# Optimization experiments

Measured on AMD Instinct MI355X. Metric: run time of the kernel, lower is better.

## Reference

```python
import jax, jax.numpy as jnp
import numpy as np

B, T, D, H, K, V, W = 2, 2048, 768, 12, 64, 64, 1024
EPS = 1e-6


def setup_inputs() -> dict:
    key = jax.random.key(0)
    ks = jax.random.split(key, 10)
    std = 0.02
    return {
        "x": jax.random.normal(ks[0], (B, T, D), jnp.float32),
        "gdn_state": jax.random.normal(ks[1], (B, H, K, V), jnp.float32),
        "Wq": jax.random.normal(ks[2], (D, H * K), jnp.float32) * std,
        "Wk": jax.random.normal(ks[3], (D, H * K), jnp.float32) * std,
        "Wv": jax.random.normal(ks[4], (D, H * K), jnp.float32) * std,
        "Wo": jax.random.normal(ks[5], (H * K, D), jnp.float32) * std,
        "Wgq": jax.random.normal(ks[6], (D, H * K), jnp.float32) * std,
        "Wro": jax.random.normal(ks[7], (H * V, D), jnp.float32) * std,
        "Wg": jax.random.normal(ks[8], (D, H), jnp.float32) * std,
        "bg": jnp.full((H,), 1.0, jnp.float32),  # swa_gate_init
        "norm_w": jnp.ones((D,), jnp.float32),
    }


def reference(x, gdn_state, Wq, Wk, Wv, Wo, Wgq, Wro, Wg, bg, norm_w):
    # RMSNorm
    xn = x * jax.lax.rsqrt(jnp.mean(x * x, axis=-1, keepdims=True) + EPS) * norm_w

    def proj(w):  # (B,T,D)@(D,HK) -> (B,H,T,K)
        return (xn @ w).reshape(B, T, H, K).transpose(0, 2, 1, 3)

    q, k, v = proj(Wq), proj(Wk), proj(Wv)
    scale = K ** -0.5

    scores = jnp.einsum("bhqk,bhsk->bhqs", q, k) * scale  # (B,H,T,T)
    i = jnp.arange(T)[:, None]
    j = jnp.arange(T)[None, :]
    allowed = (j <= i) & (j >= i - W)  # causal sliding window
    scores = jnp.where(allowed, scores, -jnp.inf)
    attn = jax.nn.softmax(scores, axis=-1)

    local = jnp.einsum("bhqs,bhsk->bhqk", attn, v)
    local = local.transpose(0, 2, 1, 3).reshape(B, T, H * K) @ Wo  # (B,T,D)

    # GDN state retrieval
    qg = jax.nn.relu((xn @ Wgq).reshape(B, T, H, K).transpose(0, 2, 1, 3))  # (B,H,T,K)
    retrieved = jnp.einsum("bhkv,bhtk->bhtv", gdn_state, qg)  # (B,H,T,V)
    retrieval = retrieved.transpose(0, 2, 1, 3).reshape(B, T, H * V) @ Wro  # (B,T,D)
    gate = jax.nn.sigmoid(xn @ Wg + bg)  # (B,T,H)
    retrieval = jnp.mean(gate, axis=-1, keepdims=True) * retrieval

    return x + local + retrieval
```

## Files before the change

### kernel.cpp

```cpp
#include <hip/hip_runtime.h>
#include <math.h>
#include <stdint.h>

typedef float f32x4 __attribute__((ext_vector_type(4)));
typedef __bf16 bf16x8 __attribute__((ext_vector_type(8)));
typedef __bf16 bf16x4 __attribute__((ext_vector_type(4)));

constexpr int Bc = 2, Tc = 2048, Dc = 768, Hc = 12, Wc = 1024;
#define CEXP 0.18033688011112042f

__device__ __forceinline__ f32x4 mfma_bf16(bf16x8 a, bf16x8 b, f32x4 c) {
    return __builtin_amdgcn_mfma_f32_16x16x32_bf16(a, b, c, 0, 0, 0);
}
__device__ __forceinline__ void gload16(const void* g, void* l) {
    __builtin_amdgcn_global_load_lds(
        (const __attribute__((address_space(1))) uint32_t*)g,
        (__attribute__((address_space(3))) uint32_t*)l, 16, 0, 0);
}
__device__ __forceinline__ uint32_t pack2(float a, float b) {
    union { __bf16 h[2]; uint32_t u; } x;
    x.h[0] = (__bf16)a; x.h[1] = (__bf16)b; return x.u;
}

__global__ __launch_bounds__(256) void k_prep_w(
    const float* __restrict__ Wq, const float* __restrict__ Wk,
    const float* __restrict__ Wv, const float* __restrict__ Wgq,
    const float* __restrict__ Wo, const float* __restrict__ Wro,
    __bf16* __restrict__ wTproj, __bf16* __restrict__ wTout)
{
    __shared__ __bf16 ldsT[64][66];
    const int wsel = blockIdx.y;
    const float* srcs[6] = {Wq, Wk, Wv, Wgq, Wo, Wro};
    const float* src = srcs[wsel];
    __bf16* dst; int dstride, koff;
    if (wsel < 4) { dst = wTproj + (size_t)wsel * Dc * Dc; dstride = Dc;  koff = 0; }
    else if (wsel == 4) { dst = wTout; dstride = 1536; koff = 0; }
    else { dst = wTout; dstride = 1536; koff = 768; }
    const float scale = (wsel == 0) ? CEXP : 1.0f;

    int tile = blockIdx.x;
    int tk = tile % 12, tn = tile / 12;
    int k0 = tk * 64, n0 = tn * 64;
    int i = threadIdx.x, rsub = i >> 4, c4 = i & 15;
#pragma unroll
    for (int rep = 0; rep < 4; ++rep) {
        int row = rep * 16 + rsub;
        float4 v = *(const float4*)(src + (size_t)(k0 + row) * Dc + n0 + c4 * 4);
        ldsT[c4 * 4 + 0][row] = (__bf16)(v.x * scale);
        ldsT[c4 * 4 + 1][row] = (__bf16)(v.y * scale);
        ldsT[c4 * 4 + 2][row] = (__bf16)(v.z * scale);
        ldsT[c4 * 4 + 3][row] = (__bf16)(v.w * scale);
    }
    __syncthreads();
#pragma unroll
    for (int rep = 0; rep < 4; ++rep) {
        int n = rep * 16 + rsub;
        bf16x4 o = *(const bf16x4*)&ldsT[n][c4 * 4];
        *(bf16x4*)(dst + (size_t)(n0 + n) * dstride + koff + k0 + c4 * 4) = o;
    }
}

__global__ __launch_bounds__(256) void k_prep_state(
    const float* __restrict__ st, __bf16* __restrict__ stT)
{
    int idx = blockIdx.x * 256 + threadIdx.x;
    int bh = idx >> 12, kk = (idx >> 6) & 63, vv = idx & 63;
    stT[(size_t)bh * 4096 + vv * 64 + kk] = (__bf16)st[idx];
}

__global__ __launch_bounds__(256) void k_rmsnorm(
    const float* __restrict__ x, const float* __restrict__ norm_w,
    __bf16* __restrict__ xnb)
{
    int row = blockIdx.x, tid = threadIdx.x;
    const float* xr = x + (size_t)row * Dc;
    float4 v = make_float4(0.f, 0.f, 0.f, 0.f);
    float ss = 0.f;
    if (tid < 192) {
        v = ((const float4*)xr)[tid];
        ss = v.x * v.x + v.y * v.y + v.z * v.z + v.w * v.w;
    }
#pragma unroll
    for (int m = 32; m; m >>= 1) ss += __shfl_xor(ss, m, 64);
    __shared__ float red[4];
    if ((tid & 63) == 0) red[tid >> 6] = ss;
    __syncthreads();
    float tot = red[0] + red[1] + red[2] + red[3];
    float rms = rsqrtf(tot * (1.f / 768.f) + 1e-6f);
    if (tid < 192) {
        float4 nw = ((const float4*)norm_w)[tid];
        bf16x4 o;
        o[0] = (__bf16)(v.x * rms * nw.x);
        o[1] = (__bf16)(v.y * rms * nw.y);
        o[2] = (__bf16)(v.z * rms * nw.z);
        o[3] = (__bf16)(v.w * rms * nw.w);
        *(bf16x4*)(xnb + (size_t)row * Dc + tid * 4) = o;
    }
}

__global__ __launch_bounds__(256) void k_gate(
    const __bf16* __restrict__ xnb, const float* __restrict__ Wg,
    const float* __restrict__ bg, float* __restrict__ gmean)
{
    int row = blockIdx.x * 4 + (threadIdx.x >> 6);
    int lane = threadIdx.x & 63;
    const __bf16* xr = xnb + (size_t)row * Dc;
    float p[12];
#pragma unroll
    for (int h = 0; h < 12; ++h) p[h] = 0.f;
    for (int d = lane; d < Dc; d += 64) {
        float xv = (float)xr[d];
        const float* wr = Wg + d * 12;
#pragma unroll
        for (int h = 0; h < 12; ++h) p[h] += xv * wr[h];
    }
#pragma unroll
    for (int h = 0; h < 12; ++h) {
#pragma unroll
        for (int m = 32; m; m >>= 1) p[h] += __shfl_xor(p[h], m, 64);
    }
    if (lane == 0) {
        float s = 0.f;
#pragma unroll
        for (int h = 0; h < 12; ++h) s += 1.f / (1.f + expf(-(p[h] + bg[h])));
        gmean[row] = s * (1.f / 12.f);
    }
}

template <int MODE>
__global__ __launch_bounds__(256) void k_gemm(
    const __bf16* __restrict__ A, const __bf16* __restrict__ BT,
    const float* __restrict__ xres, float* __restrict__ outf,
    __bf16* __restrict__ qb, __bf16* __restrict__ kbf,
    __bf16* __restrict__ vtb, __bf16* __restrict__ qgb)
{
    constexpr int BM = (MODE == 0) ? 128 : 64;
    constexpr int BN = (MODE == 0) ? 128 : 64;
    constexpr int KD = (MODE == 0) ? 768 : 1536;
    constexpr int WM = BM / 2, WN = BN / 2;
    constexpr int MI = WM / 16, NI = WN / 16;
    constexpr int MT = 4096 / BM;
    __shared__ __bf16 As[BM * 32];
    __shared__ __bf16 Bs[BN * 32];
    const int tid = threadIdx.x, w = tid >> 6, lane = tid & 63;
    const int g = lane >> 4, t = lane & 15;
    int id = blockIdx.x, xcd = id & 7, l = id >> 3;
    int nid = xcd * 96 + l;
    int m0 = (nid % MT) * BM, n0 = (nid / MT) * BN;
    const __bf16* Abase = A + (size_t)m0 * KD;
    const __bf16* Bbase = BT + (size_t)n0 * KD;
    const int wrow = (w >> 1) * WM, wcol = (w & 1) * WN;

    f32x4 acc[MI][NI] = {};
    for (int k0 = 0; k0 < KD; k0 += 32) {
#pragma unroll
        for (int c = 0; c < BM / 64; ++c) {
            int chunk = c * 256 + tid, row = chunk >> 2, cix = chunk & 3;
            gload16(Abase + (size_t)row * KD + k0 + cix * 8, As + chunk * 8);
        }
#pragma unroll
        for (int c = 0; c < BN / 64; ++c) {
            int chunk = c * 256 + tid, row = chunk >> 2, cix = chunk & 3;
            gload16(Bbase + (size_t)row * KD + k0 + cix * 8, Bs + chunk * 8);
        }
        __syncthreads();
        bf16x8 af[MI], bfr[NI];
#pragma unroll
        for (int mi = 0; mi < MI; ++mi)
            af[mi] = *(const bf16x8*)(As + (wrow + mi * 16 + t) * 32 + g * 8);
#pragma unroll
        for (int ni = 0; ni < NI; ++ni)
            bfr[ni] = *(const bf16x8*)(Bs + (wcol + ni * 16 + t) * 32 + g * 8);
#pragma unroll
        for (int mi = 0; mi < MI; ++mi)
#pragma unroll
            for (int ni = 0; ni < NI; ++ni)
                acc[mi][ni] = mfma_bf16(af[mi], bfr[ni], acc[mi][ni]);
        __syncthreads();
    }
    const int region = (MODE == 0) ? (n0 / 768) : 0;
#pragma unroll
    for (int mi = 0; mi < MI; ++mi)
#pragma unroll
        for (int ni = 0; ni < NI; ++ni)
#pragma unroll
            for (int r = 0; r < 4; ++r) {
                int grow = m0 + wrow + mi * 16 + g * 4 + r;
                int gcol = n0 + wcol + ni * 16 + t;
                float v = acc[mi][ni][r];
                if (MODE == 1) {
                    size_t idx = (size_t)grow * Dc + gcol;
                    outf[idx] = xres[idx] + v;
                } else {
                    int c = gcol - region * 768;
                    int h = c >> 6, kd = c & 63;
                    int b = grow >> 11, ti = grow & (Tc - 1);
                    if (region == 0)
                        qb[((size_t)(b * Hc + h) * Tc + ti) * 64 + kd] = (__bf16)v;
                    else if (region == 1) {
                        int kds = kd ^ ((ti & 7) << 3);
                        kbf[((size_t)(b * Hc + h) * Tc + ti) * 64 + kds] = (__bf16)v;
                    } else if (region == 2) {
                        int ts = (ti & ~63) | ((ti & 63) ^ ((kd & 7) << 3));
                        vtb[((size_t)(b * Hc + h) * 64 + kd) * Tc + ts] = (__bf16)v;
                    } else
                        qgb[((size_t)(b * Hc + h) * Tc + ti) * 64 + kd] = (__bf16)fmaxf(v, 0.f);
                }
            }
}

__global__ __launch_bounds__(256) void k_attn(
    const __bf16* __restrict__ q, const __bf16* __restrict__ k,
    const __bf16* __restrict__ vt, __bf16* __restrict__ ac)
{
    __shared__ __bf16 Ks[2][64 * 64];
    __shared__ __bf16 Vs[2][64 * 64];
    int id = blockIdx.x, xcd = id & 7, l = id >> 3;
    int nid = xcd * 96 + l;
    int sblk = nid & 31, h = (nid >> 5) % Hc, b = nid / (32 * Hc);
    int tid = threadIdx.x;
    int w = tid >> 6, lane = tid & 63;
    int g = lane >> 4, t = lane & 15;
    int q0 = sblk * 64, qw = q0 + w * 16;
    const __bf16* qb = q + (size_t)(b * Hc + h) * Tc * 64;
    const __bf16* kb = k + (size_t)(b * Hc + h) * Tc * 64;
    const __bf16* vb = vt + (size_t)(b * Hc + h) * 64 * Tc;

    bf16x8 qf0 = *(const bf16x8*)(qb + (size_t)(qw + t) * 64 + g * 8);
    bf16x8 qf1 = *(const bf16x8*)(qb + (size_t)(qw + t) * 64 + 32 + g * 8);

    const int qi = qw + t;
    const int lowB = qi - Wc;
    const int xr = t & 7;

    f32x4 oacc[4] = {};
    float lsum = 0.f;

    const int s_begin = (q0 >= Wc) ? q0 - Wc : 0;
    const int s_endq = q0 + 64;

    auto STAGE = [&](int buf, int s0) {
#pragma unroll
        for (int j = 0; j < 2; ++j) {
            int ch = j * 256 + tid;
            gload16(kb + (size_t)(s0 + (ch >> 3)) * 64 + (ch & 7) * 8,
                    &Ks[buf][ch * 8]);
            gload16(vb + (size_t)(ch >> 3) * Tc + s0 + (ch & 7) * 8,
                    &Vs[buf][ch * 8]);
        }
    };

    STAGE(0, s_begin);
    __syncthreads();
    int cur = 0;
    for (int s0 = s_begin; s0 < s_endq; s0 += 64) {
        if (s0 + 64 < s_endq) STAGE(cur ^ 1, s0 + 64);
        const __bf16* Kt = Ks[cur];
        const __bf16* Vt = Vs[cur];
        f32x4 sc[4];
#pragma unroll
        for (int sub = 0; sub < 4; ++sub) {
            const __bf16* kr = Kt + (sub * 16 + t) * 64;
            bf16x8 kA = *(const bf16x8*)(kr + ((g ^ xr) << 3));
            bf16x8 kB = *(const bf16x8*)(kr + (((g + 4) ^ xr) << 3));
            f32x4 s = {};
            s = mfma_bf16(kA, qf0, s);
            s = mfma_bf16(kB, qf1, s);
            sc[sub] = s;
        }
        float pv[4][4];
#pragma unroll
        for (int sub = 0; sub < 4; ++sub)
#pragma unroll
            for (int r = 0; r < 4; ++r) {
                int kk = s0 + sub * 16 + g * 4 + r;
                float e = exp2f(sc[sub][r]);
                float val = (kk <= qi && kk >= lowB) ? e : 0.f;
                pv[sub][r] = val;
                lsum += val;
            }
#pragma unroll
        for (int ks = 0; ks < 2; ++ks) {
            const float* p0 = pv[ks * 2];
            const float* p1 = pv[ks * 2 + 1];
            uint32_t u0 = pack2(p0[0], p0[1]), u1 = pack2(p0[2], p0[3]);
            uint32_t u2 = pack2(p1[0], p1[1]), u3 = pack2(p1[2], p1[3]);
            int srcA = (g & 1) * 32 + t, srcB = srcA + 16;
            uint32_t a0 = __shfl(u0, srcA, 64), a1 = __shfl(u1, srcA, 64);
            uint32_t a2 = __shfl(u0, srcB, 64), a3 = __shfl(u1, srcB, 64);
            uint32_t c0 = __shfl(u2, srcA, 64), c1 = __shfl(u3, srcA, 64);
            uint32_t c2 = __shfl(u2, srcB, 64), c3 = __shfl(u3, srcB, 64);
            bool lo2 = g < 2;
            union { uint32_t u[4]; bf16x8 v; } pf;
            pf.u[0] = lo2 ? a0 : c0; pf.u[1] = lo2 ? a1 : c1;
            pf.u[2] = lo2 ? a2 : c2; pf.u[3] = lo2 ? a3 : c3;
#pragma unroll
            for (int n = 0; n < 4; ++n) {
                const __bf16* vrow = Vt + (n * 16 + t) * 64;
                bf16x8 vf = *(const bf16x8*)(vrow + ((((ks * 4) + g) ^ xr) << 3));
                oacc[n] = mfma_bf16(pf.v, vf, oacc[n]);
            }
        }
        __syncthreads();
        cur ^= 1;
    }
    lsum += __shfl_xor(lsum, 16, 64);
    lsum += __shfl_xor(lsum, 32, 64);
    float linv = 1.f / lsum;
    float lq[4];
#pragma unroll
    for (int r = 0; r < 4; ++r) lq[r] = __shfl(linv, g * 4 + r, 64);
#pragma unroll
    for (int n = 0; n < 4; ++n)
#pragma unroll
        for (int r = 0; r < 4; ++r) {
            int qrow = qw + g * 4 + r;
            ac[(size_t)(b * Tc + qrow) * 1536 + h * 64 + n * 16 + t] =
                (__bf16)(oacc[n][r] * lq[r]);
        }
}

__global__ __launch_bounds__(256) void k_retr(
    const __bf16* __restrict__ qg, const __bf16* __restrict__ stateT,
    const float* __restrict__ gmean, __bf16* __restrict__ ac)
{
    int b = blockIdx.z, h = blockIdx.y;
    int w = threadIdx.x >> 6, lane = threadIdx.x & 63;
    int g = lane >> 4, t = lane & 15;
    int t0 = blockIdx.x * 64 + w * 16;
    const __bf16* qbp = qg + (size_t)(b * Hc + h) * Tc * 64;
    const __bf16* sb = stateT + (size_t)(b * Hc + h) * 64 * 64;
    bf16x8 a0 = *(const bf16x8*)(qbp + (size_t)(t0 + t) * 64 + g * 8);
    bf16x8 a1 = *(const bf16x8*)(qbp + (size_t)(t0 + t) * 64 + 32 + g * 8);
#pragma unroll
    for (int n = 0; n < 4; ++n) {
        bf16x8 b0 = *(const bf16x8*)(sb + (n * 16 + t) * 64 + g * 8);
        bf16x8 b1 = *(const bf16x8*)(sb + (n * 16 + t) * 64 + 32 + g * 8);
        f32x4 acc = {};
        acc = mfma_bf16(a0, b0, acc);
        acc = mfma_bf16(a1, b1, acc);
#pragma unroll
        for (int r = 0; r < 4; ++r) {
            int ti = t0 + g * 4 + r;
            float gm = gmean[b * Tc + ti];
            ac[(size_t)(b * Tc + ti) * 1536 + 768 + h * 64 + n * 16 + t] =
                (__bf16)(acc[r] * gm);
        }
    }
}

extern "C" void kernel_launch(void* const* d_in, const int* in_sizes, int n_in,
                              void* d_out, int out_size, void* d_ws, size_t ws_size,
                              hipStream_t stream) {
    (void)in_sizes; (void)n_in; (void)out_size; (void)ws_size;
    const float* x     = (const float*)d_in[0];
    const float* gdn   = (const float*)d_in[1];
    const float* Wq    = (const float*)d_in[2];
    const float* Wk    = (const float*)d_in[3];
    const float* Wv    = (const float*)d_in[4];
    const float* Wo    = (const float*)d_in[5];
    const float* Wgq   = (const float*)d_in[6];
    const float* Wro   = (const float*)d_in[7];
    const float* Wg    = (const float*)d_in[8];
    const float* bg    = (const float*)d_in[9];
    const float* normw = (const float*)d_in[10];
    float* out = (float*)d_out;

    char* p = (char*)d_ws;
    auto alloc = [&](size_t bytes) -> char* {
        char* r = p; p += (bytes + 255) & ~(size_t)255; return r;
    };
    constexpr size_t NROW = (size_t)Bc * Tc;
    __bf16* xnb    = (__bf16*)alloc(NROW * Dc * 2);
    __bf16* wTproj = (__bf16*)alloc((size_t)4 * Dc * Dc * 2);
    __bf16* wTout  = (__bf16*)alloc((size_t)Dc * 1536 * 2);
    __bf16* stT    = (__bf16*)alloc((size_t)Bc * Hc * 64 * 64 * 2);
    __bf16* qbuf   = (__bf16*)alloc(NROW * Dc * 2);
    __bf16* kbuf   = (__bf16*)alloc(NROW * Dc * 2);
    __bf16* qgbuf  = (__bf16*)alloc(NROW * Dc * 2);
    __bf16* vtbuf  = (__bf16*)alloc(NROW * Dc * 2);
    __bf16* ac     = (__bf16*)alloc(NROW * 1536 * 2);
    float*  gmean  = (float*)alloc(NROW * 4);

    k_prep_w<<<dim3(144, 6), 256, 0, stream>>>(Wq, Wk, Wv, Wgq, Wo, Wro, wTproj, wTout);
    k_prep_state<<<(Bc * Hc * 64 * 64) / 256, 256, 0, stream>>>(gdn, stT);
    k_rmsnorm<<<NROW, 256, 0, stream>>>(x, normw, xnb);
    k_gate<<<NROW / 4, 256, 0, stream>>>(xnb, Wg, bg, gmean);

    k_gemm<0><<<768, 256, 0, stream>>>(xnb, wTproj, nullptr, nullptr,
                                       qbuf, kbuf, vtbuf, qgbuf);
    k_attn<<<768, 256, 0, stream>>>(qbuf, kbuf, vtbuf, ac);
    k_retr<<<dim3(Tc / 64, Hc, Bc), 256, 0, stream>>>(qgbuf, stT, gmean, ac);
    k_gemm<1><<<768, 256, 0, stream>>>(ac, wTout, x, out,
                                       nullptr, nullptr, nullptr, nullptr);
}
```

Measured before the change: 140.4 us.

## Widen GEMM K-tile with swizzled LDS and permute V layout to drop shuffles

The GEMM K-step doubles from 32 to 64, with an XOR swizzle on the LDS chunk placement to avoid bank conflicts, which halves the number of barrier pairs per tile. The V-transpose store layout gains an extra permutation of the time index so that the attention kernel's P fragments match the MFMA operand layout directly. That lets the per-step cross-lane shuffles for P be dropped. LDS use per GEMM block doubles, and correctness depends on the permutation exactly matching the MFMA lane mapping.

Result: no change. 137.7 us (-2.0%).

```diff
diff --git a/kernel.cpp b/kernel.cpp
--- a/kernel.cpp
+++ b/kernel.cpp
@@ -140,8 +140,8 @@
     constexpr int WM = BM / 2, WN = BN / 2;
     constexpr int MI = WM / 16, NI = WN / 16;
     constexpr int MT = 4096 / BM;
-    __shared__ __bf16 As[BM * 32];
-    __shared__ __bf16 Bs[BN * 32];
+    __shared__ __bf16 As[BM * 64];
+    __shared__ __bf16 Bs[BN * 64];
     const int tid = threadIdx.x, w = tid >> 6, lane = tid & 63;
     const int g = lane >> 4, t = lane & 15;
     int id = blockIdx.x, xcd = id & 7, l = id >> 3;
@@ -150,32 +150,40 @@
     const __bf16* Abase = A + (size_t)m0 * KD;
     const __bf16* Bbase = BT + (size_t)n0 * KD;
     const int wrow = (w >> 1) * WM, wcol = (w & 1) * WN;
+    const int xr = t & 7;
 
     f32x4 acc[MI][NI] = {};
-    for (int k0 = 0; k0 < KD; k0 += 32) {
-#pragma unroll
-        for (int c = 0; c < BM / 64; ++c) {
-            int chunk = c * 256 + tid, row = chunk >> 2, cix = chunk & 3;
-            gload16(Abase + (size_t)row * KD + k0 + cix * 8, As + chunk * 8);
-        }
-#pragma unroll
-        for (int c = 0; c < BN / 64; ++c) {
-            int chunk = c * 256 + tid, row = chunk >> 2, cix = chunk & 3;
-            gload16(Bbase + (size_t)row * KD + k0 + cix * 8, Bs + chunk * 8);
+    for (int k0 = 0; k0 < KD; k0 += 64) {
+#pragma unroll
+        for (int c = 0; c < BM / 32; ++c) {
+            int chunk = c * 256 + tid, row = chunk >> 3, cix = chunk & 7;
+            gload16(Abase + (size_t)row * KD + k0 + ((cix ^ (row & 7)) << 3),
+                    As + chunk * 8);
+        }
+#pragma unroll
+        for (int c = 0; c < BN / 32; ++c) {
+            int chunk = c * 256 + tid, row = chunk >> 3, cix = chunk & 7;
+            gload16(Bbase + (size_t)row * KD + k0 + ((cix ^ (row & 7)) << 3),
+                    Bs + chunk * 8);
         }
         __syncthreads();
-        bf16x8 af[MI], bfr[NI];
-#pragma unroll
-        for (int mi = 0; mi < MI; ++mi)
-            af[mi] = *(const bf16x8*)(As + (wrow + mi * 16 + t) * 32 + g * 8);
-#pragma unroll
-        for (int ni = 0; ni < NI; ++ni)
-            bfr[ni] = *(const bf16x8*)(Bs + (wcol + ni * 16 + t) * 32 + g * 8);
-#pragma unroll
-        for (int mi = 0; mi < MI; ++mi)
+#pragma unroll
+        for (int kk = 0; kk < 2; ++kk) {
+            bf16x8 af[MI], bfr[NI];
+#pragma unroll
+            for (int mi = 0; mi < MI; ++mi)
+                af[mi] = *(const bf16x8*)(As + (wrow + mi * 16 + t) * 64 +
+                                          (((g + kk * 4) ^ xr) << 3));
 #pragma unroll
             for (int ni = 0; ni < NI; ++ni)
-                acc[mi][ni] = mfma_bf16(af[mi], bfr[ni], acc[mi][ni]);
+                bfr[ni] = *(const bf16x8*)(Bs + (wcol + ni * 16 + t) * 64 +
+                                           (((g + kk * 4) ^ xr) << 3));
+#pragma unroll
+            for (int mi = 0; mi < MI; ++mi)
+#pragma unroll
+                for (int ni = 0; ni < NI; ++ni)
+                    acc[mi][ni] = mfma_bf16(af[mi], bfr[ni], acc[mi][ni]);
+        }
         __syncthreads();
     }
     const int region = (MODE == 0) ? (n0 / 768) : 0;
@@ -201,7 +209,10 @@
                         int kds = kd ^ ((ti & 7) << 3);
                         kbf[((size_t)(b * Hc + h) * Tc + ti) * 64 + kds] = (__bf16)v;
                     } else if (region == 2) {
-                        int ts = (ti & ~63) | ((ti & 63) ^ ((kd & 7) << 3));
+                        int kap = ti & 63;
+                        int rho = (kap & 32) | (((kap >> 2) & 3) << 3) |
+                                  (((kap >> 4) & 1) << 2) | (kap & 3);
+                        int ts = (ti & ~63) | (rho ^ ((kd & 7) << 3));
                         vtb[((size_t)(b * Hc + h) * 64 + kd) * Tc + ts] = (__bf16)v;
                     } else
                         qgb[((size_t)(b * Hc + h) * Tc + ti) * 64 + kd] = (__bf16)fmaxf(v, 0.f);
@@ -281,19 +292,11 @@
             }
 #pragma unroll
         for (int ks = 0; ks < 2; ++ks) {
-            const float* p0 = pv[ks * 2];
-            const float* p1 = pv[ks * 2 + 1];
-            uint32_t u0 = pack2(p0[0], p0[1]), u1 = pack2(p0[2], p0[3]);
-            uint32_t u2 = pack2(p1[0], p1[1]), u3 = pack2(p1[2], p1[3]);
-            int srcA = (g & 1) * 32 + t, srcB = srcA + 16;
-            uint32_t a0 = __shfl(u0, srcA, 64), a1 = __shfl(u1, srcA, 64);
-            uint32_t a2 = __shfl(u0, srcB, 64), a3 = __shfl(u1, srcB, 64);
-            uint32_t c0 = __shfl(u2, srcA, 64), c1 = __shfl(u3, srcA, 64);
-            uint32_t c2 = __shfl(u2, srcB, 64), c3 = __shfl(u3, srcB, 64);
-            bool lo2 = g < 2;
             union { uint32_t u[4]; bf16x8 v; } pf;
-            pf.u[0] = lo2 ? a0 : c0; pf.u[1] = lo2 ? a1 : c1;
-            pf.u[2] = lo2 ? a2 : c2; pf.u[3] = lo2 ? a3 : c3;
+            pf.u[0] = pack2(pv[ks * 2][0], pv[ks * 2][1]);
+            pf.u[1] = pack2(pv[ks * 2][2], pv[ks * 2][3]);
+            pf.u[2] = pack2(pv[ks * 2 + 1][0], pv[ks * 2 + 1][1]);
+            pf.u[3] = pack2(pv[ks * 2 + 1][2], pv[ks * 2 + 1][3]);
 #pragma unroll
             for (int n = 0; n < 4; ++n) {
                 const __bf16* vrow = Vt + (n * 16 + t) * 64;
```
